# Kernel tuning notes

Hardware: AMD Instinct MI355X
Metric: run time of the kernel (lower is better)

The kernel has to match this reference:

```python
import jax, jax.numpy as jnp
import numpy as np

DIM = 1024
N_HEADS = 16
HEAD_DIM = DIM // N_HEADS
HIDDEN = 4096  # round_up(4*DIM, 256)
ROPE_THETA = 10000.0
EPS = 1e-6


def setup_inputs() -> dict:
    key = jax.random.key(0)
    ks = jax.random.split(key, 10)
    s = 0.02
    return {
        "x": jax.random.normal(ks[0], (1, 4096, DIM), dtype=jnp.float32),
        "wq": jax.random.normal(ks[1], (DIM, DIM), dtype=jnp.float32) * s,
        "wk": jax.random.normal(ks[2], (DIM, DIM), dtype=jnp.float32) * s,
        "wv": jax.random.normal(ks[3], (DIM, DIM), dtype=jnp.float32) * s,
        "wo": jax.random.normal(ks[4], (DIM, DIM), dtype=jnp.float32) * s,
        "w1": jax.random.normal(ks[5], (HIDDEN, DIM), dtype=jnp.float32) * s,
        "w2": jax.random.normal(ks[6], (DIM, HIDDEN), dtype=jnp.float32) * s,
        "w3": jax.random.normal(ks[7], (HIDDEN, DIM), dtype=jnp.float32) * s,
        "g_attn": jnp.ones((DIM,), dtype=jnp.float32),
        "g_ffn": jnp.ones((DIM,), dtype=jnp.float32),
    }


def _rmsnorm(x, g):
    return x * jax.lax.rsqrt(jnp.mean(x * x, axis=-1, keepdims=True) + EPS) * g


def _rope_tables(seqlen):
    inv = 1.0 / (ROPE_THETA ** (jnp.arange(0, HEAD_DIM, 2, dtype=jnp.float32) / HEAD_DIM))
    ang = jnp.arange(seqlen, dtype=jnp.float32)[:, None] * inv[None, :]  # [s, hd/2]
    return jnp.cos(ang), jnp.sin(ang)


def _apply_rope(q, cos, sin):
    # q: [b, s, h, hd]; pairs (even, odd) treated as complex (re, im)
    b, s, h, d = q.shape
    qr = q.reshape(b, s, h, d // 2, 2)
    re, im = qr[..., 0], qr[..., 1]
    c = cos[None, :, None, :]
    sn = sin[None, :, None, :]
    out = jnp.stack([re * c - im * sn, re * sn + im * c], axis=-1)
    return out.reshape(b, s, h, d)


def reference(x, wq, wk, wv, wo, w1, w2, w3, g_attn, g_ffn):
    b, s, _ = x.shape
    xn = _rmsnorm(x, g_attn)
    q = (xn @ wq.T).reshape(b, s, N_HEADS, HEAD_DIM)
    k = (xn @ wk.T).reshape(b, s, N_HEADS, HEAD_DIM)
    v = (xn @ wv.T).reshape(b, s, N_HEADS, HEAD_DIM)
    cos, sin = _rope_tables(s)
    q = _apply_rope(q, cos, sin)
    k = _apply_rope(k, cos, sin)
    scores = jnp.einsum("bthd,bThd->bhtT", q, k) / np.sqrt(HEAD_DIM).astype(np.float32)
    probs = jax.nn.softmax(scores, axis=-1)
    attn = jnp.einsum("bhtT,bThd->bthd", probs, v).reshape(b, s, DIM)
    h = x + attn @ wo.T
    hn = _rmsnorm(h, g_ffn)
    ff = (jax.nn.silu(hn @ w1.T) * (hn @ w3.T)) @ w2.T
    return h + ff
```

## Files before the change

### kernel.cpp

```cpp
#include <hip/hip_runtime.h>

#define S_LEN 4096
#define DIMM  1024
#define NH    16
#define HD    64
#define HID   4096

typedef unsigned short u16;
typedef __attribute__((ext_vector_type(8))) short bf16x8;
typedef __attribute__((ext_vector_type(4))) short short4b;
typedef __attribute__((ext_vector_type(8))) unsigned short u16x8;
typedef __attribute__((ext_vector_type(4))) float f32x4;

__device__ __forceinline__ u16 f2bf(float f) {
  unsigned u = __float_as_uint(f);
  u += 0x7fffu + ((u >> 16) & 1u);
  return (u16)(u >> 16);
}
__device__ __forceinline__ float bf2f(u16 h) {
  return __uint_as_float(((unsigned)h) << 16);
}
__device__ __forceinline__ unsigned pack_bf16(float hi, float lo) {
  return __builtin_amdgcn_perm(__float_as_uint(hi), __float_as_uint(lo), 0x07060302u);
}
__device__ __forceinline__ float fexp2(float x) { return __builtin_amdgcn_exp2f(x); }

__device__ __forceinline__ void gl_lds16(const void* g, void* l) {
  __builtin_amdgcn_global_load_lds(
      (const __attribute__((address_space(1))) void*)g,
      (__attribute__((address_space(3))) void*)l, 16, 0, 0);
}

__device__ __forceinline__ f32x4 mfma16(short4b a, short4b b, f32x4 c) {
#if __has_builtin(__builtin_amdgcn_mfma_f32_16x16x16bf16_1k)
  return __builtin_amdgcn_mfma_f32_16x16x16bf16_1k(a, b, c, 0, 0, 0);
#else
  asm("v_mfma_f32_16x16x16_bf16 %0, %1, %2, %0" : "+v"(c) : "v"(a), "v"(b));
  return c;
#endif
}

__global__ __launch_bounds__(256) void prep_kernel(
    const float* __restrict__ wq, const float* __restrict__ wk, const float* __restrict__ wv,
    const float* __restrict__ wo, const float* __restrict__ w1, const float* __restrict__ w3,
    const float* __restrict__ w2, const float* __restrict__ x, const float* __restrict__ g_attn,
    u16* __restrict__ wqkb, u16* __restrict__ wvb, u16* __restrict__ wob,
    u16* __restrict__ w13b, u16* __restrict__ w2b, u16* __restrict__ xnb,
    float* __restrict__ cosT, float* __restrict__ sinT) {
  int b = blockIdx.x;
  int t = threadIdx.x;
  if (b < 8192) {
    const float* src;
    u16* dst;
    int i;
    if (b < 2048) {
      int which = b >> 9, lb = b & 511;
      src = which == 0 ? wq : which == 1 ? wk : which == 2 ? wv : wo;
      dst = which == 0 ? wqkb : which == 1 ? (wqkb + (1 << 20)) : which == 2 ? wvb : wob;
      i = (lb * 256 + t) * 8;
    } else {
      int b2 = b - 2048, which = b2 >> 11, lb = b2 & 2047;
      src = which == 0 ? w1 : which == 1 ? w3 : w2;
      dst = which == 0 ? w13b : which == 1 ? (w13b + (4 << 20)) : w2b;
      i = (lb * 256 + t) * 8;
    }
    float4 a = *(const float4*)(src + i);
    float4 c = *(const float4*)(src + i + 4);
    u16x8 r;
    r[0] = f2bf(a.x); r[1] = f2bf(a.y); r[2] = f2bf(a.z); r[3] = f2bf(a.w);
    r[4] = f2bf(c.x); r[5] = f2bf(c.y); r[6] = f2bf(c.z); r[7] = f2bf(c.w);
    *(u16x8*)(dst + i) = r;
  } else if (b < 8704) {
    int idx = (b - 8192) * 256 + t;
    int pos = idx >> 5, i = idx & 31;
    double inv = pow(10000.0, -(double)(2 * i) / 64.0);
    double a = (double)pos * inv;
    cosT[idx] = (float)cos(a);
    sinT[idx] = (float)sin(a);
  } else {
    int row = b - 8704;
    const float4 v = *(const float4*)(x + (size_t)row * DIMM + t * 4);
    float ss = v.x * v.x + v.y * v.y + v.z * v.z + v.w * v.w;
#pragma unroll
    for (int off = 32; off > 0; off >>= 1) ss += __shfl_down(ss, off);
    __shared__ float red[4];
    if ((t & 63) == 0) red[t >> 6] = ss;
    __syncthreads();
    float tot = red[0] + red[1] + red[2] + red[3];
    float sc = rsqrtf(tot * (1.0f / DIMM) + 1e-6f);
    const float4 gv = *(const float4*)(g_attn + t * 4);
    ushort4 o;
    o.x = f2bf(v.x * sc * gv.x);
    o.y = f2bf(v.y * sc * gv.y);
    o.z = f2bf(v.z * sc * gv.z);
    o.w = f2bf(v.w * sc * gv.w);
    *(ushort4*)(xnb + (size_t)row * DIMM + t * 4) = o;
  }
}

__global__ __launch_bounds__(256) void rmsnorm_kernel(const float* __restrict__ x, const float* __restrict__ g,
                                                      u16* __restrict__ out) {
  int row = blockIdx.x;
  int t = threadIdx.x;
  const float4 v = *(const float4*)(x + (size_t)row * DIMM + t * 4);
  float ss = v.x * v.x + v.y * v.y + v.z * v.z + v.w * v.w;
#pragma unroll
  for (int off = 32; off > 0; off >>= 1) ss += __shfl_down(ss, off);
  __shared__ float red[4];
  if ((t & 63) == 0) red[t >> 6] = ss;
  __syncthreads();
  float tot = red[0] + red[1] + red[2] + red[3];
  float sc = rsqrtf(tot * (1.0f / DIMM) + 1e-6f);
  const float4 gv = *(const float4*)(g + t * 4);
  ushort4 o;
  o.x = f2bf(v.x * sc * gv.x);
  o.y = f2bf(v.y * sc * gv.y);
  o.z = f2bf(v.z * sc * gv.z);
  o.w = f2bf(v.w * sc * gv.w);
  *(ushort4*)(out + (size_t)row * DIMM + t * 4) = o;
}

template <int OUTMODE>
__global__ __launch_bounds__(512) void gemm_kernel(const u16* __restrict__ A, const u16* __restrict__ B,
                                                   void* Cout, const float* res, int N, int K, int lda,
                                                   const float* cosT, const float* sinT) {
  __shared__ uint4 As0[1024], Bs0[1024], As1[1024], Bs1[1024];
  const int t = threadIdx.x;
  const int w = t >> 6, l = t & 63;
  const int wm = w >> 1, wn = w & 1;
  const int bm = blockIdx.y, bn = blockIdx.x;
  const int quad = l >> 4, lc = l & 15;

  f32x4 acc[2][4];
  const f32x4 zero = {0.0f, 0.0f, 0.0f, 0.0f};
#pragma unroll
  for (int mi = 0; mi < 2; mi++)
#pragma unroll
    for (int ni = 0; ni < 4; ni++) acc[mi][ni] = zero;

  const int band0 = t >> 6, kq0 = (t >> 4) & 3, row0 = t & 15;
  const u16* Ap0 = A + (size_t)(bm * 128 + band0 * 16 + row0) * lda + kq0 * 8;
  const u16* Bp0 = B + (size_t)(bn * 128 + band0 * 16 + row0) * K + kq0 * 8;
  const int abase = wm * 128 + l;
  const int bbase = wn * 256 + l;

#define STAGEL(AD, BD, K0)                 \
  do {                                     \
    gl_lds16(Ap0 + (K0), &(AD)[t]);        \
    gl_lds16(Ap0 + (K0) + 32, &(AD)[t + 512]); \
    gl_lds16(Bp0 + (K0), &(BD)[t]);        \
    gl_lds16(Bp0 + (K0) + 32, &(BD)[t + 512]); \
  } while (0)

#define COMPL(AS, BS)                                                                               \
  do {                                                                                              \
    _Pragma("unroll") for (int ks = 0; ks < 2; ks++) {                                              \
      bf16x8 af[2], bfr[4];                                                                         \
      _Pragma("unroll") for (int mi = 0; mi < 2; mi++)                                              \
          af[mi] = *(const bf16x8*)&(AS)[ks * 512 + abase + mi * 64];                               \
      _Pragma("unroll") for (int ni = 0; ni < 4; ni++)                                              \
          bfr[ni] = *(const bf16x8*)&(BS)[ks * 512 + bbase + ni * 64];                              \
      _Pragma("unroll") for (int mi = 0; mi < 2; mi++)                                              \
          _Pragma("unroll") for (int ni = 0; ni < 4; ni++)                                          \
              acc[mi][ni] = __builtin_amdgcn_mfma_f32_16x16x32_bf16(af[mi], bfr[ni], acc[mi][ni], 0, 0, 0); \
    }                                                                                               \
  } while (0)

  STAGEL(As0, Bs0, 0);
  __syncthreads();
  int k0 = 0;
  for (; k0 + 128 < K; k0 += 128) {
    STAGEL(As1, Bs1, k0 + 64);
    COMPL(As0, Bs0);
    __syncthreads();
    STAGEL(As0, Bs0, k0 + 128);
    COMPL(As1, Bs1);
    __syncthreads();
  }
  STAGEL(As1, Bs1, k0 + 64);
  COMPL(As0, Bs0);
  __syncthreads();
  COMPL(As1, Bs1);
#undef STAGEL
#undef COMPL

  const int rbase = bm * 128 + wm * 32 + quad * 4;
  const int cbase = bn * 128 + wn * 64 + lc;
  const float qs = (OUTMODE == 3 && bn < 8) ? 0.18033688011112f : 1.0f;
#pragma unroll
  for (int mi = 0; mi < 2; mi++) {
#pragma unroll
    for (int r = 0; r < 4; r++) {
      int row = rbase + mi * 16 + r;
#pragma unroll
      for (int ni = 0; ni < 4; ni++) {
        int col = cbase + ni * 16;
        if constexpr (OUTMODE == 0) {
          ((u16*)Cout)[(size_t)row * N + col] = f2bf(acc[mi][ni][r]);
        } else if constexpr (OUTMODE == 1) {
          size_t idx = (size_t)row * N + col;
          ((float*)Cout)[idx] = res[idx] + acc[mi][ni][r];
        } else if constexpr (OUTMODE == 2) {
          int h = row >> 6, din = row & 63;
          int kb = col >> 6, k63 = col & 63;
          int off = ((h << 6) + kb) * 4096 + (((din >> 4) << 1) + (k63 >> 5)) * 512 +
                    ((((k63 >> 2) & 3) << 4) + (din & 15)) * 8 + ((k63 >> 4) & 1) * 4 + (k63 & 3);
          ((u16*)Cout)[off] = f2bf(acc[mi][ni][r]);
        } else {
          float v = acc[mi][ni][r];
          float pv = __shfl_xor(v, 1);
          int i = ((ni * 16 + lc) & 63) >> 1;
          float c = cosT[(row << 5) + i], s = sinT[(row << 5) + i];
          float o = (lc & 1) ? (pv * s + v * c) : (v * c - pv * s);
          ((u16*)Cout)[(size_t)row * N + col] = f2bf(o * qs);
        }
      }
    }
  }
}

__global__ __launch_bounds__(512) void gemm256_kernel(const u16* __restrict__ A, const u16* __restrict__ B,
                                                      u16* __restrict__ Cout, int N, int K, int lda) {
  __shared__ uint4 As0[1024], Bs0[1024], As1[1024], Bs1[1024];
  const int t = threadIdx.x;
  const int w = t >> 6, l = t & 63;
  const int wm = w >> 2, wn = w & 3;
  const int bm = blockIdx.y, bn = blockIdx.x;
  const int quad = l >> 4, lc = l & 15;

  f32x4 acc[8][4];
  const f32x4 zero = {0.0f, 0.0f, 0.0f, 0.0f};
#pragma unroll
  for (int mi = 0; mi < 8; mi++)
#pragma unroll
    for (int ni = 0; ni < 4; ni++) acc[mi][ni] = zero;

  const int band0 = t >> 6, kq0 = (t >> 4) & 3, row0 = t & 15;
  const u16* Ap0 = A + (size_t)(bm * 256 + band0 * 16 + row0) * lda + kq0 * 8;
  const u16* Bp0 = B + (size_t)(bn * 256 + band0 * 16 + row0) * K + kq0 * 8;
  const size_t Astep = (size_t)128 * lda;
  const size_t Bstep = (size_t)128 * K;

#define STAGE256(AD, BD, K0)                      \
  do {                                            \
    gl_lds16(Ap0 + (K0), &(AD)[t]);               \
    gl_lds16(Ap0 + Astep + (K0), &(AD)[t + 512]); \
    gl_lds16(Bp0 + (K0), &(BD)[t]);               \
    gl_lds16(Bp0 + Bstep + (K0), &(BD)[t + 512]); \
  } while (0)

#define COMPUTE256(AS, BS)                                                                          \
  do {                                                                                              \
    bf16x8 af[8], bfr[4];                                                                           \
    _Pragma("unroll") for (int mi = 0; mi < 8; mi++)                                                \
        af[mi] = *(const bf16x8*)&(AS)[(wm * 8 + mi) * 64 + l];                                     \
    _Pragma("unroll") for (int ni = 0; ni < 4; ni++)                                                \
        bfr[ni] = *(const bf16x8*)&(BS)[(wn * 4 + ni) * 64 + l];                                    \
    _Pragma("unroll") for (int mi = 0; mi < 8; mi++)                                                \
        _Pragma("unroll") for (int ni = 0; ni < 4; ni++)                                            \
            acc[mi][ni] = __builtin_amdgcn_mfma_f32_16x16x32_bf16(af[mi], bfr[ni], acc[mi][ni], 0, 0, 0); \
  } while (0)

  STAGE256(As0, Bs0, 0);
  __syncthreads();

  int k0 = 0;
  for (; k0 + 64 < K; k0 += 64) {
    STAGE256(As1, Bs1, k0 + 32);
    COMPUTE256(As0, Bs0);
    __syncthreads();
    STAGE256(As0, Bs0, k0 + 64);
    COMPUTE256(As1, Bs1);
    __syncthreads();
  }
  STAGE256(As1, Bs1, k0 + 32);
  COMPUTE256(As0, Bs0);
  __syncthreads();
  COMPUTE256(As1, Bs1);
#undef STAGE256
#undef COMPUTE256

  const int rbase = bm * 256 + wm * 128 + quad * 4;
  const int cbase = bn * 256 + wn * 64 + lc;
#pragma unroll
  for (int mi = 0; mi < 8; mi++) {
#pragma unroll
    for (int r = 0; r < 4; r++) {
      int row = rbase + mi * 16 + r;
#pragma unroll
      for (int ni = 0; ni < 4; ni++) {
        int col = cbase + ni * 16;
        Cout[(size_t)row * N + col] = f2bf(acc[mi][ni][r]);
      }
    }
  }
}

__global__ __launch_bounds__(512) void attn_kernel(const u16* __restrict__ Qm, const u16* __restrict__ Km,
                                                   const u16* __restrict__ Vsw, u16* __restrict__ Om) {
  __shared__ char smem[32768];
  uint4* Ks0 = (uint4*)smem;
  uint4* Vs0 = (uint4*)(smem + 8192);
  uint4* Ks1 = (uint4*)(smem + 16384);
  uint4* Vs1 = (uint4*)(smem + 24576);
  const int t = threadIdx.x;
  const int w = t >> 6, l = t & 63;
  const int quad = l >> 4, lc = l & 15;
  const int hd = blockIdx.y;
  const int qrow = blockIdx.x * 128 + w * 16;

  bf16x8 qf_[2];
#pragma unroll
  for (int ch = 0; ch < 2; ch++)
    qf_[ch] = *(const bf16x8*)(Qm + (size_t)(qrow + lc) * 2048 + hd * HD + ch * 32 + quad * 8);

  const f32x4 zero = {0.0f, 0.0f, 0.0f, 0.0f};
  const short4b ones4 = {(short)0x3F80, (short)0x3F80, (short)0x3F80, (short)0x3F80};
  f32x4 Oa[4];
#pragma unroll
  for (int df = 0; df < 4; df++) Oa[df] = zero;
  f32x4 lsacc = zero;
  float mt = -1e30f;

  const int s0 = t >> 7, c0 = (t >> 6) & 1, kq0 = (t >> 4) & 3, row0 = t & 15;
  const u16* Kp0 = Km + (size_t)(s0 * 16 + row0) * 2048 + hd * HD + c0 * 32 + kq0 * 8;
  const u16* Vp = Vsw + (size_t)(hd * HD) * 4096 + t * 8;

#define STAGEKV(KD, VD, TT)                                  \
  do {                                                       \
    gl_lds16(Kp0 + (size_t)(TT)*131072, &(KD)[t]);           \
    gl_lds16(Vp + (size_t)(TT)*4096, &(VD)[t]);              \
  } while (0)

#define TILE_COMPUTE(KS, VS)                                                                 \
  do {                                                                                       \
    f32x4 Sf[4];                                                                             \
    _Pragma("unroll") for (int kf = 0; kf < 4; kf++) {                                       \
      bf16x8 ka = *(const bf16x8*)&(KS)[kf * 128 + l];                                       \
      bf16x8 kb2 = *(const bf16x8*)&(KS)[kf * 128 + 64 + l];                                 \
      f32x4 z = __builtin_amdgcn_mfma_f32_16x16x32_bf16(ka, qf_[0], zero, 0, 0, 0);          \
      z = __builtin_amdgcn_mfma_f32_16x16x32_bf16(kb2, qf_[1], z, 0, 0, 0);                  \
      Sf[kf] = z;                                                                            \
    }                                                                                        \
    float tmax = -1e30f;                                                                     \
    _Pragma("unroll") for (int kf = 0; kf < 4; kf++)                                         \
        _Pragma("unroll") for (int r = 0; r < 4; r++) tmax = fmaxf(tmax, Sf[kf][r]);         \
    tmax = fmaxf(tmax, __shfl_xor(tmax, 16));                                                \
    tmax = fmaxf(tmax, __shfl_xor(tmax, 32));                                                \
    if (!__all(tmax <= mt + 8.0f)) {                                                        \
      float mnew = fmaxf(mt, tmax);                                                          \
      float alpha = fexp2(mt - mnew);                                                        \
      mt = mnew;                                                                             \
      lsacc *= alpha;                                                                        \
      _Pragma("unroll") for (int df = 0; df < 4; df++) Oa[df] *= alpha;                      \
    }                                                                                        \
    _Pragma("unroll") for (int kf = 0; kf < 4; kf++)                                         \
        _Pragma("unroll") for (int r = 0; r < 4; r++)                                        \
      Sf[kf][r] = fexp2(Sf[kf][r] - mt);                                                     \
    short4b pk[4];                                                                           \
    _Pragma("unroll") for (int kf = 0; kf < 4; kf++) {                                       \
      union { short4b s4; uint2 u2; } cv;                                                    \
      cv.u2.x = pack_bf16(Sf[kf][1], Sf[kf][0]);                                             \
      cv.u2.y = pack_bf16(Sf[kf][3], Sf[kf][2]);                                             \
      pk[kf] = cv.s4;                                                                        \
    }                                                                                        \
    _Pragma("unroll") for (int kf = 0; kf < 4; kf++)                                         \
      lsacc = mfma16(ones4, pk[kf], lsacc);                                                  \
    _Pragma("unroll") for (int df = 0; df < 4; df++)                                         \
        _Pragma("unroll") for (int tp = 0; tp < 2; tp++) {                                   \
      union { bf16x8 v8; short4b h[2]; } vv;                                                 \
      vv.v8 = *(const bf16x8*)&(VS)[(df * 2 + tp) * 64 + l];                                 \
      Oa[df] = mfma16(vv.h[0], pk[2 * tp], Oa[df]);                                          \
      Oa[df] = mfma16(vv.h[1], pk[2 * tp + 1], Oa[df]);                                      \
    }                                                                                        \
  } while (0)

  STAGEKV(Ks0, Vs0, 0);
  __syncthreads();

  for (int tt = 0; tt < 64; tt += 2) {
    STAGEKV(Ks1, Vs1, tt + 1);
    TILE_COMPUTE(Ks0, Vs0);
    __syncthreads();
    if (tt + 2 < 64) STAGEKV(Ks0, Vs0, tt + 2);
    TILE_COMPUTE(Ks1, Vs1);
    __syncthreads();
  }
#undef STAGEKV
#undef TILE_COMPUTE

  u16* ep = (u16*)smem;
  float invl = 1.0f / lsacc[0];
#pragma unroll
  for (int df = 0; df < 4; df++) {
    int qb = w * 16 + lc;
    int d = df * 16 + quad * 4;
    uint2 pv;
    pv.x = pack_bf16(Oa[df][1] * invl, Oa[df][0] * invl);
    pv.y = pack_bf16(Oa[df][3] * invl, Oa[df][2] * invl);
    *(uint2*)(ep + qb * 72 + d) = pv;
  }
  __syncthreads();
#pragma unroll
  for (int it = 0; it < 2; it++) {
    int qb = it * 64 + (t >> 3);
    int dp = (t & 7) * 8;
    u16x8 rowv = *(const u16x8*)(ep + qb * 72 + dp);
    *(u16x8*)(Om + (size_t)(blockIdx.x * 128 + qb) * DIMM + hd * HD + dp) = rowv;
  }
}

__global__ __launch_bounds__(256) void silu_mul_kernel(u16* __restrict__ u13) {
  int i = (blockIdx.x * 256 + threadIdx.x) * 8;
  int r = i >> 12, c = i & 4095;
  u16* up = u13 + (size_t)r * 8192 + c;
  u16x8 uv = *(const u16x8*)up;
  u16x8 gv = *(const u16x8*)(up + 4096);
  u16x8 o;
#pragma unroll
  for (int j = 0; j < 8; j++) {
    float a = bf2f(uv[j]);
    float b = bf2f(gv[j]);
    float sv = a / (1.0f + __expf(-a));
    o[j] = f2bf(sv * b);
  }
  *(u16x8*)up = o;
}

extern "C" void kernel_launch(void* const* d_in, const int* in_sizes, int n_in,
                              void* d_out, int out_size, void* d_ws, size_t ws_size,
                              hipStream_t stream) {
  const float* x      = (const float*)d_in[0];
  const float* wq     = (const float*)d_in[1];
  const float* wk     = (const float*)d_in[2];
  const float* wv     = (const float*)d_in[3];
  const float* wo     = (const float*)d_in[4];
  const float* w1     = (const float*)d_in[5];
  const float* w2     = (const float*)d_in[6];
  const float* w3     = (const float*)d_in[7];
  const float* g_attn = (const float*)d_in[8];
  const float* g_ffn  = (const float*)d_in[9];
  float* out = (float*)d_out;
  char* ws = (char*)d_ws;
  const size_t MB = 1ull << 20;

  u16* wqkb = (u16*)(ws + 0 * MB);
  u16* wvb  = (u16*)(ws + 4 * MB);
  u16* wob  = (u16*)(ws + 6 * MB);
  u16* w13b = (u16*)(ws + 8 * MB);
  u16* w2b  = (u16*)(ws + 24 * MB);
  u16* xnb  = (u16*)(ws + 32 * MB);
  u16* qkb  = (u16*)(ws + 40 * MB);
  u16* vswz = (u16*)(ws + 56 * MB);
  u16* attb = (u16*)(ws + 64 * MB);
  u16* u13  = (u16*)(ws + 40 * MB);
  float* cosT = (float*)(ws + 104 * MB);
  float* sinT = (float*)(ws + 104 * MB + 512 * 1024);

  prep_kernel<<<12800, 256, 0, stream>>>(wq, wk, wv, wo, w1, w3, w2, x, g_attn,
                                         wqkb, wvb, wob, w13b, w2b, xnb, cosT, sinT);

  gemm_kernel<3><<<dim3(16, 32), 512, 0, stream>>>(xnb, wqkb, qkb, nullptr, 2048, DIMM, DIMM, cosT, sinT);
  gemm_kernel<2><<<dim3(32, 8), 512, 0, stream>>>(wvb, xnb, vswz, nullptr, S_LEN, DIMM, DIMM, nullptr, nullptr);

  attn_kernel<<<dim3(32, 16), 512, 0, stream>>>(qkb, qkb + 1024, vswz, attb);

  gemm_kernel<1><<<dim3(8, 32), 512, 0, stream>>>(attb, wob, out, x, DIMM, DIMM, DIMM, nullptr, nullptr);

  rmsnorm_kernel<<<4096, 256, 0, stream>>>(out, g_ffn, xnb);

  gemm256_kernel<<<dim3(32, 16), 512, 0, stream>>>(xnb, w13b, u13, 8192, DIMM, DIMM);

  silu_mul_kernel<<<8192, 256, 0, stream>>>(u13);

  gemm_kernel<1><<<dim3(8, 32), 512, 0, stream>>>(u13, w2b, out, out, DIMM, HID, 8192, nullptr, nullptr);
}
```

Baseline: 529.8 us.

## Restructure gemm256 pipeline with 64-wide K tiles and prefetch two ahead

The 256x256 GEMM now stages 64-wide K tiles, each tile holding two 32-wide halves, into double buffers. Each iteration reads all fragments into registers, barriers once, issues the global-to-LDS prefetch for tile tt+2 into the buffer it just drained, then runs the MFMAs at raised priority. Explicit vmcnt/lgkmcnt waits replace the previous pair of __syncthreads per 64 K. This doubles LDS use to 128 KB per block and keeps more loads in flight, which may limit occupancy. It also depends on manual waitcnt accounting being correct.

```diff
diff --git a/kernel.cpp b/kernel.cpp
--- a/kernel.cpp
+++ b/kernel.cpp
@@ -221,7 +221,7 @@
 
 __global__ __launch_bounds__(512) void gemm256_kernel(const u16* __restrict__ A, const u16* __restrict__ B,
                                                       u16* __restrict__ Cout, int N, int K, int lda) {
-  __shared__ uint4 As0[1024], Bs0[1024], As1[1024], Bs1[1024];
+  __shared__ uint4 As0[2048], Bs0[2048], As1[2048], Bs1[2048];
   const int t = threadIdx.x;
   const int w = t >> 6, l = t & 63;
   const int wm = w >> 2, wn = w & 3;
@@ -241,44 +241,63 @@
   const size_t Astep = (size_t)128 * lda;
   const size_t Bstep = (size_t)128 * K;
 
-#define STAGE256(AD, BD, K0)                      \
-  do {                                            \
-    gl_lds16(Ap0 + (K0), &(AD)[t]);               \
-    gl_lds16(Ap0 + Astep + (K0), &(AD)[t + 512]); \
-    gl_lds16(Bp0 + (K0), &(BD)[t]);               \
-    gl_lds16(Bp0 + Bstep + (K0), &(BD)[t + 512]); \
+#define STG(AD, BD, K0)                                \
+  do {                                                 \
+    gl_lds16(Ap0 + (K0), &(AD)[t]);                    \
+    gl_lds16(Ap0 + Astep + (K0), &(AD)[t + 512]);      \
+    gl_lds16(Ap0 + (K0) + 32, &(AD)[t + 1024]);        \
+    gl_lds16(Ap0 + Astep + (K0) + 32, &(AD)[t + 1536]);\
+    gl_lds16(Bp0 + (K0), &(BD)[t]);                    \
+    gl_lds16(Bp0 + Bstep + (K0), &(BD)[t + 512]);      \
+    gl_lds16(Bp0 + (K0) + 32, &(BD)[t + 1024]);        \
+    gl_lds16(Bp0 + Bstep + (K0) + 32, &(BD)[t + 1536]);\
   } while (0)
 
-#define COMPUTE256(AS, BS)                                                                          \
-  do {                                                                                              \
-    bf16x8 af[8], bfr[4];                                                                           \
-    _Pragma("unroll") for (int mi = 0; mi < 8; mi++)                                                \
-        af[mi] = *(const bf16x8*)&(AS)[(wm * 8 + mi) * 64 + l];                                     \
-    _Pragma("unroll") for (int ni = 0; ni < 4; ni++)                                                \
-        bfr[ni] = *(const bf16x8*)&(BS)[(wn * 4 + ni) * 64 + l];                                    \
-    _Pragma("unroll") for (int mi = 0; mi < 8; mi++)                                                \
-        _Pragma("unroll") for (int ni = 0; ni < 4; ni++)                                            \
-            acc[mi][ni] = __builtin_amdgcn_mfma_f32_16x16x32_bf16(af[mi], bfr[ni], acc[mi][ni], 0, 0, 0); \
-  } while (0)
-
-  STAGE256(As0, Bs0, 0);
-  __syncthreads();
-
-  int k0 = 0;
-  for (; k0 + 64 < K; k0 += 64) {
-    STAGE256(As1, Bs1, k0 + 32);
-    COMPUTE256(As0, Bs0);
-    __syncthreads();
-    STAGE256(As0, Bs0, k0 + 64);
-    COMPUTE256(As1, Bs1);
-    __syncthreads();
-  }
-  STAGE256(As1, Bs1, k0 + 32);
-  COMPUTE256(As0, Bs0);
-  __syncthreads();
-  COMPUTE256(As1, Bs1);
-#undef STAGE256
-#undef COMPUTE256
+  const int NT = K >> 6;
+  STG(As0, Bs0, 0);
+  STG(As1, Bs1, 64);
+  asm volatile("s_waitcnt vmcnt(8)" ::: "memory");
+  __builtin_amdgcn_s_barrier();
+
+  for (int tt = 0; tt < NT; ++tt) {
+    const uint4* AS = (tt & 1) ? As1 : As0;
+    const uint4* BS = (tt & 1) ? Bs1 : Bs0;
+    uint4* ASd = (tt & 1) ? As1 : As0;
+    uint4* BSd = (tt & 1) ? Bs1 : Bs0;
+
+    bf16x8 af[2][8], bfr[2][4];
+#pragma unroll
+    for (int ks = 0; ks < 2; ks++) {
+#pragma unroll
+      for (int mi = 0; mi < 8; mi++)
+        af[ks][mi] = *(const bf16x8*)&AS[ks * 1024 + (wm * 8 + mi) * 64 + l];
+#pragma unroll
+      for (int ni = 0; ni < 4; ni++)
+        bfr[ks][ni] = *(const bf16x8*)&BS[ks * 1024 + (wn * 4 + ni) * 64 + l];
+    }
+    asm volatile("s_waitcnt lgkmcnt(0)" ::: "memory");
+    __builtin_amdgcn_s_barrier();
+
+    if (tt + 2 < NT) STG(ASd, BSd, (tt + 2) * 64);
+
+    __builtin_amdgcn_s_setprio(1);
+#pragma unroll
+    for (int ks = 0; ks < 2; ks++)
+#pragma unroll
+      for (int mi = 0; mi < 8; mi++)
+#pragma unroll
+        for (int ni = 0; ni < 4; ni++)
+          acc[mi][ni] = __builtin_amdgcn_mfma_f32_16x16x32_bf16(af[ks][mi], bfr[ks][ni], acc[mi][ni], 0, 0, 0);
+    __builtin_amdgcn_s_setprio(0);
+
+    if (tt + 2 < NT) {
+      asm volatile("s_waitcnt vmcnt(8)" ::: "memory");
+    } else if (tt + 1 < NT) {
+      asm volatile("s_waitcnt vmcnt(0)" ::: "memory");
+    }
+    if (tt + 1 < NT) __builtin_amdgcn_s_barrier();
+  }
+#undef STG
 
   const int rbase = bm * 256 + wm * 128 + quad * 4;
   const int cbase = bn * 256 + wn * 64 + lc;
```

Result: faster. 512.9 us (-3.2%).

## Software-pipeline GEMM main loop with register-prefetched fragments and explicit waitcnts

Applied to the files above, without the earlier changes.

Restructures the 256x256 bf16 GEMM K-loop so that the LDS fragments for the next K-slice are read into a second register set while the MFMAs for the current slice run. Full __syncthreads calls are replaced by explicit vmcnt/lgkmcnt waits plus raw s_barrier, and s_setprio is raised around the MFMA block to favour matrix issue. The aim is to hide LDS-read and global-to-LDS latency behind MFMA work. The cost is a second set of fragment registers, which raises register pressure, and more fragile hand-managed synchronization.

```diff
diff --git a/kernel.cpp b/kernel.cpp
--- a/kernel.cpp
+++ b/kernel.cpp
@@ -241,7 +241,7 @@
   const size_t Astep = (size_t)128 * lda;
   const size_t Bstep = (size_t)128 * K;
 
-#define STAGE256(AD, BD, K0)                      \
+#define STG(AD, BD, K0)                           \
   do {                                            \
     gl_lds16(Ap0 + (K0), &(AD)[t]);               \
     gl_lds16(Ap0 + Astep + (K0), &(AD)[t + 512]); \
@@ -249,36 +249,53 @@
     gl_lds16(Bp0 + Bstep + (K0), &(BD)[t + 512]); \
   } while (0)
 
-#define COMPUTE256(AS, BS)                                                                          \
+#define READF(AF, BF, AS, BS)                                                    \
+  do {                                                                           \
+    _Pragma("unroll") for (int mi = 0; mi < 8; mi++)                             \
+        AF[mi] = *(const bf16x8*)&(AS)[(wm * 8 + mi) * 64 + l];                  \
+    _Pragma("unroll") for (int ni = 0; ni < 4; ni++)                             \
+        BF[ni] = *(const bf16x8*)&(BS)[(wn * 4 + ni) * 64 + l];                  \
+  } while (0)
+
+#define MM(AF, BF)                                                                                  \
   do {                                                                                              \
-    bf16x8 af[8], bfr[4];                                                                           \
-    _Pragma("unroll") for (int mi = 0; mi < 8; mi++)                                                \
-        af[mi] = *(const bf16x8*)&(AS)[(wm * 8 + mi) * 64 + l];                                     \
-    _Pragma("unroll") for (int ni = 0; ni < 4; ni++)                                                \
-        bfr[ni] = *(const bf16x8*)&(BS)[(wn * 4 + ni) * 64 + l];                                    \
     _Pragma("unroll") for (int mi = 0; mi < 8; mi++)                                                \
         _Pragma("unroll") for (int ni = 0; ni < 4; ni++)                                            \
-            acc[mi][ni] = __builtin_amdgcn_mfma_f32_16x16x32_bf16(af[mi], bfr[ni], acc[mi][ni], 0, 0, 0); \
-  } while (0)
-
-  STAGE256(As0, Bs0, 0);
-  __syncthreads();
-
-  int k0 = 0;
-  for (; k0 + 64 < K; k0 += 64) {
-    STAGE256(As1, Bs1, k0 + 32);
-    COMPUTE256(As0, Bs0);
-    __syncthreads();
-    STAGE256(As0, Bs0, k0 + 64);
-    COMPUTE256(As1, Bs1);
-    __syncthreads();
-  }
-  STAGE256(As1, Bs1, k0 + 32);
-  COMPUTE256(As0, Bs0);
-  __syncthreads();
-  COMPUTE256(As1, Bs1);
-#undef STAGE256
-#undef COMPUTE256
+            acc[mi][ni] = __builtin_amdgcn_mfma_f32_16x16x32_bf16(AF[mi], BF[ni], acc[mi][ni], 0, 0, 0); \
+  } while (0)
+
+  bf16x8 afA[8], bfA[4], afB[8], bfB[4];
+  const int NT = K >> 5;
+
+  STG(As0, Bs0, 0);
+  STG(As1, Bs1, 32);
+  asm volatile("s_waitcnt vmcnt(4)" ::: "memory");
+  __builtin_amdgcn_s_barrier();
+  READF(afA, bfA, As0, Bs0);
+  asm volatile("s_waitcnt lgkmcnt(0)" ::: "memory");
+
+  for (int tt = 0; tt < NT; tt += 2) {
+    asm volatile("s_waitcnt vmcnt(0)" ::: "memory");
+    __builtin_amdgcn_s_barrier();
+    if (tt + 2 < NT) STG(As0, Bs0, (tt + 2) * 32);
+    READF(afB, bfB, As1, Bs1);
+    __builtin_amdgcn_s_setprio(1);
+    MM(afA, bfA);
+    __builtin_amdgcn_s_setprio(0);
+    asm volatile("s_waitcnt lgkmcnt(0)" ::: "memory");
+
+    asm volatile("s_waitcnt vmcnt(0)" ::: "memory");
+    __builtin_amdgcn_s_barrier();
+    if (tt + 3 < NT) STG(As1, Bs1, (tt + 3) * 32);
+    if (tt + 2 < NT) READF(afA, bfA, As0, Bs0);
+    __builtin_amdgcn_s_setprio(1);
+    MM(afB, bfB);
+    __builtin_amdgcn_s_setprio(0);
+    asm volatile("s_waitcnt lgkmcnt(0)" ::: "memory");
+  }
+#undef STG
+#undef READF
+#undef MM
 
   const int rbase = bm * 256 + wm * 128 + quad * 4;
   const int cbase = bn * 256 + wn * 64 + lc;
```

Measured after the change: 534.6 us. No clear change (+0.9%).

## Triple-buffer gemm256 LDS staging with partial vmcnt waits and MFMA priority

Applied to the files above, without the earlier changes.

The 256x256 GEMM kernel moves from a double-buffered to a triple-buffered LDS pipeline. Each tile is prefetched two steps ahead, and a partial vmcnt wait replaces the full __syncthreads, so global loads for the next tiles can stay in flight while MFMAs run. s_setprio is raised around the MFMA block to favour compute-issuing waves. LDS use grows from 64KB to 96KB per block, and correctness depends on the hand-placed waitcnt and barrier ordering.

```diff
diff --git a/kernel.cpp b/kernel.cpp
--- a/kernel.cpp
+++ b/kernel.cpp
@@ -221,7 +221,7 @@
 
 __global__ __launch_bounds__(512) void gemm256_kernel(const u16* __restrict__ A, const u16* __restrict__ B,
                                                       u16* __restrict__ Cout, int N, int K, int lda) {
-  __shared__ uint4 As0[1024], Bs0[1024], As1[1024], Bs1[1024];
+  __shared__ uint4 As0[1024], Bs0[1024], As1[1024], Bs1[1024], As2[1024], Bs2[1024];
   const int t = threadIdx.x;
   const int w = t >> 6, l = t & 63;
   const int wm = w >> 2, wn = w & 3;
@@ -241,7 +241,7 @@
   const size_t Astep = (size_t)128 * lda;
   const size_t Bstep = (size_t)128 * K;
 
-#define STAGE256(AD, BD, K0)                      \
+#define STG(AD, BD, K0)                           \
   do {                                            \
     gl_lds16(Ap0 + (K0), &(AD)[t]);               \
     gl_lds16(Ap0 + Astep + (K0), &(AD)[t + 512]); \
@@ -249,36 +249,44 @@
     gl_lds16(Bp0 + Bstep + (K0), &(BD)[t + 512]); \
   } while (0)
 
-#define COMPUTE256(AS, BS)                                                                          \
-  do {                                                                                              \
-    bf16x8 af[8], bfr[4];                                                                           \
-    _Pragma("unroll") for (int mi = 0; mi < 8; mi++)                                                \
-        af[mi] = *(const bf16x8*)&(AS)[(wm * 8 + mi) * 64 + l];                                     \
-    _Pragma("unroll") for (int ni = 0; ni < 4; ni++)                                                \
-        bfr[ni] = *(const bf16x8*)&(BS)[(wn * 4 + ni) * 64 + l];                                    \
-    _Pragma("unroll") for (int mi = 0; mi < 8; mi++)                                                \
-        _Pragma("unroll") for (int ni = 0; ni < 4; ni++)                                            \
+  const int NT = K >> 5;
+
+#define PHASE(CA, CB, SA, SB, TT)                                              \
+  do {                                                                         \
+    if ((TT) + 2 < NT) STG(SA, SB, ((TT) + 2) * 32);                           \
+    bf16x8 af[8], bfr[4];                                                      \
+    _Pragma("unroll") for (int mi = 0; mi < 8; mi++)                           \
+        af[mi] = *(const bf16x8*)&(CA)[(wm * 8 + mi) * 64 + l];                \
+    _Pragma("unroll") for (int ni = 0; ni < 4; ni++)                           \
+        bfr[ni] = *(const bf16x8*)&(CB)[(wn * 4 + ni) * 64 + l];               \
+    __builtin_amdgcn_s_setprio(1);                                             \
+    _Pragma("unroll") for (int mi = 0; mi < 8; mi++)                           \
+        _Pragma("unroll") for (int ni = 0; ni < 4; ni++)                       \
             acc[mi][ni] = __builtin_amdgcn_mfma_f32_16x16x32_bf16(af[mi], bfr[ni], acc[mi][ni], 0, 0, 0); \
-  } while (0)
-
-  STAGE256(As0, Bs0, 0);
-  __syncthreads();
-
-  int k0 = 0;
-  for (; k0 + 64 < K; k0 += 64) {
-    STAGE256(As1, Bs1, k0 + 32);
-    COMPUTE256(As0, Bs0);
-    __syncthreads();
-    STAGE256(As0, Bs0, k0 + 64);
-    COMPUTE256(As1, Bs1);
-    __syncthreads();
-  }
-  STAGE256(As1, Bs1, k0 + 32);
-  COMPUTE256(As0, Bs0);
-  __syncthreads();
-  COMPUTE256(As1, Bs1);
-#undef STAGE256
-#undef COMPUTE256
+    __builtin_amdgcn_s_setprio(0);                                             \
+    if ((TT) + 1 < NT) {                                                       \
+      asm volatile("s_waitcnt lgkmcnt(0)" ::: "memory");                       \
+      if ((TT) + 2 < NT) {                                                     \
+        asm volatile("s_waitcnt vmcnt(4)" ::: "memory");                       \
+      } else {                                                                 \
+        asm volatile("s_waitcnt vmcnt(0)" ::: "memory");                       \
+      }                                                                        \
+      __builtin_amdgcn_s_barrier();                                            \
+    }                                                                          \
+  } while (0)
+
+  STG(As0, Bs0, 0);
+  STG(As1, Bs1, 32);
+  asm volatile("s_waitcnt vmcnt(4)" ::: "memory");
+  __builtin_amdgcn_s_barrier();
+
+  for (int tt = 0; tt < NT; tt += 3) {
+    PHASE(As0, Bs0, As2, Bs2, tt);
+    if (tt + 1 < NT) PHASE(As1, Bs1, As0, Bs0, tt + 1);
+    if (tt + 2 < NT) PHASE(As2, Bs2, As1, Bs1, tt + 2);
+  }
+#undef STG
+#undef PHASE
 
   const int rbase = bm * 256 + wm * 128 + quad * 4;
   const int cbase = bn * 256 + wn * 64 + lc;
```

New measurement: 516.1 us. 1.03x faster.
